# Optimization experiments

Measured on AMD Instinct MI355X. Metric: run time of the kernel, lower is better.

The kernel has to match this reference:

```python
import jax, jax.numpy as jnp
import numpy as np

B, S, D, H = 4, 2048, 1024, 16
HD = D // H

def setup_inputs() -> dict:
    key = jax.random.key(0)
    ks = jax.random.split(key, 11)
    s = 1.0 / np.sqrt(D)
    return {
        "q": jax.random.normal(ks[0], (B, S, D), jnp.float32),
        "k": jax.random.normal(ks[1], (B, S, D), jnp.float32),
        "v": jax.random.normal(ks[2], (B, S, D), jnp.float32),
        "Wq": jax.random.normal(ks[3], (D, D), jnp.float32) * s,
        "bq": jax.random.normal(ks[4], (D,), jnp.float32) * 0.01,
        "Wk": jax.random.normal(ks[5], (D, D), jnp.float32) * s,
        "bk": jax.random.normal(ks[6], (D,), jnp.float32) * 0.01,
        "Wv": jax.random.normal(ks[7], (D, D), jnp.float32) * s,
        "bv": jax.random.normal(ks[8], (D,), jnp.float32) * 0.01,
        "Wo": jax.random.normal(ks[9], (D, D), jnp.float32) * s,
        "bo": jax.random.normal(ks[10], (D,), jnp.float32) * 0.01,
    }

def reference(q, k, v, Wq, bq, Wk, bk, Wv, bv, Wo, bo):
    # linear projections + ReLU activation (as in the torch module)
    qh = jax.nn.relu(q @ Wq.T + bq)
    kh = jax.nn.relu(k @ Wk.T + bk)
    vh = jax.nn.relu(v @ Wv.T + bv)
    # split heads: [B,S,D] -> [B,H,S,HD]
    def split(x):
        return x.reshape(B, S, H, HD).transpose(0, 2, 1, 3)
    qh, kh, vh = split(qh), split(kh), split(vh)
    scale = 1.0 / np.sqrt(HD).astype(np.float32)
    scores = jnp.einsum("bhqd,bhkd->bhqk", qh, kh) * scale
    attn = jax.nn.softmax(scores, axis=-1)
    y = jnp.einsum("bhqk,bhkd->bhqd", attn, vh)
    # merge heads: [B,H,S,HD] -> [B,S,D]
    y = y.transpose(0, 2, 1, 3).reshape(B, S, D)
    return jax.nn.relu(y @ Wo.T + bo)
```

## Files before the change

kernel.cpp:

```cpp
#include <hip/hip_runtime.h>
#include <hip/hip_bf16.h>
#include <cstdint>
#include <cstddef>

#define Bc 4
#define Sc 2048
#define Dc 1024
#define Hc 16

typedef __bf16 bf16;
typedef bf16  bf16x4 __attribute__((ext_vector_type(4)));
typedef bf16  bf16x8 __attribute__((ext_vector_type(8)));
typedef float f32x4  __attribute__((ext_vector_type(4)));

__device__ __forceinline__ void load_lds16(const bf16* g, bf16* l) {
    __builtin_amdgcn_global_load_lds((const __attribute__((address_space(1))) void*)g,
                                     (__attribute__((address_space(3))) void*)l,
                                     16, 0, 0);
}

__device__ __forceinline__ void cvt16(const float* __restrict__ g,
                                      bf16x8& lo, bf16x8& hi) {
    const f32x4 a0 = *(const f32x4*)(g);
    const f32x4 a1 = *(const f32x4*)(g + 4);
    const f32x4 a2 = *(const f32x4*)(g + 8);
    const f32x4 a3 = *(const f32x4*)(g + 12);
#pragma unroll
    for (int j = 0; j < 4; j++) {
        lo[j]     = (bf16)a0[j];
        lo[j + 4] = (bf16)a1[j];
        hi[j]     = (bf16)a2[j];
        hi[j + 4] = (bf16)a3[j];
    }
}

__device__ __forceinline__ void store_relu(float* p, float v) { *p = fmaxf(v, 0.0f); }
__device__ __forceinline__ void store_relu(bf16*  p, float v) { *p = (bf16)fmaxf(v, 0.0f); }

__global__ __launch_bounds__(256)
void cvt_f32_bf16(const float* __restrict__ src, bf16* __restrict__ dst, int n16) {
    const int idx = blockIdx.x * 256 + threadIdx.x;
    if (idx >= n16) return;
    bf16x8 lo, hi;
    cvt16(src + (size_t)idx * 16, lo, hi);
    *(bf16x8*)(dst + (size_t)idx * 16)     = lo;
    *(bf16x8*)(dst + (size_t)idx * 16 + 8) = hi;
}

__global__ __launch_bounds__(256)
void cvt_w4(const float* __restrict__ s0, const float* __restrict__ s1,
            const float* __restrict__ s2, const float* __restrict__ s3,
            bf16* __restrict__ dst) {
    const float* srcs[4] = {s0, s1, s2, s3};
    const float* src = srcs[blockIdx.y];
    const int idx = blockIdx.x * 256 + threadIdx.x;
    bf16x8 lo, hi;
    cvt16(src + (size_t)idx * 16, lo, hi);
    bf16* d = dst + (size_t)blockIdx.y * ((size_t)Dc * Dc) + (size_t)idx * 16;
    *(bf16x8*)d       = lo;
    *(bf16x8*)(d + 8) = hi;
}

#define BM 128
#define BN 64
#define BK 64

template <typename TC, bool TR>
__global__ __launch_bounds__(256)
void gemm_bb(const bf16* __restrict__ A, const bf16* __restrict__ W,
             const float* __restrict__ bias, TC* __restrict__ C,
             int M, int N, int K) {
    __shared__ __align__(16) char pool[24576];
    bf16* lA = (bf16*)pool;
    bf16* lB = (bf16*)(pool + 16384);

    const int t    = threadIdx.x;
    const int lane = t & 63;
    const int wave = t >> 6;
    const int l15  = lane & 15;
    const int quad = lane >> 4;

    const int m0 = blockIdx.x * BM;
    const int n0 = blockIdx.y * BN;
    const int wm = (wave >> 1) * 64;
    const int wn = (wave & 1) * 32;

    f32x4 acc[4][2] = {};

    const int srow = t >> 3;
    const int cg   = (((t & 7) ^ (srow & 7)) << 3);
    const bf16* gA = A + (size_t)(m0 + srow) * K + cg;
    const bf16* gW = W + (size_t)(n0 + srow) * K + cg;
    bf16* lA0 = lA + t * 8;
    bf16* lB0 = lB + t * 8;

    for (int k0 = 0; k0 < K; k0 += BK) {
        __syncthreads();
#pragma unroll
        for (int c = 0; c < 4; c++)
            load_lds16(gA + (size_t)(32 * c) * K, lA0 + c * 2048);
#pragma unroll
        for (int c = 0; c < 2; c++)
            load_lds16(gW + (size_t)(32 * c) * K, lB0 + c * 2048);
        gA += BK; gW += BK;
        __syncthreads();

#pragma unroll
        for (int ks = 0; ks < 2; ks++) {
            bf16x8 af[4], bfr[2];
            const int colp = ((((ks << 2) | quad) ^ (l15 & 7)) << 3);
#pragma unroll
            for (int mt = 0; mt < 4; mt++) {
                const int row = wm + mt * 16 + l15;
                af[mt] = *(const bf16x8*)(lA + row * BK + colp);
            }
#pragma unroll
            for (int nt = 0; nt < 2; nt++) {
                const int row = wn + nt * 16 + l15;
                bfr[nt] = *(const bf16x8*)(lB + row * BK + colp);
            }
#pragma unroll
            for (int mt = 0; mt < 4; mt++)
#pragma unroll
                for (int nt = 0; nt < 2; nt++)
                    acc[mt][nt] = __builtin_amdgcn_mfma_f32_16x16x32_bf16(
                        af[mt], bfr[nt], acc[mt][nt], 0, 0, 0);
        }
    }

    if constexpr (!TR) {
#pragma unroll
        for (int nt = 0; nt < 2; nt++) {
            const int col = n0 + wn + nt * 16 + l15;
            const float bv = bias[col];
#pragma unroll
            for (int mt = 0; mt < 4; mt++) {
                const int rowb = m0 + wm + mt * 16 + quad * 4;
#pragma unroll
                for (int i = 0; i < 4; i++)
                    store_relu(&C[(size_t)(rowb + i) * N + col], acc[mt][nt][i] + bv);
            }
        }
    } else {
        __syncthreads();
        bf16* trp = (bf16*)pool;
#pragma unroll
        for (int nt = 0; nt < 2; nt++) {
            const int col = n0 + wn + nt * 16 + l15;
            const float bv = bias[col];
#pragma unroll
            for (int mt = 0; mt < 4; mt++)
#pragma unroll
                for (int i = 0; i < 4; i++)
                    trp[((wave * 32) + nt * 16 + l15) * 72 + mt * 16 + quad * 4 + i] =
                        (bf16)fmaxf(acc[mt][nt][i] + bv, 0.0f);
        }
        __syncthreads();
        const int r2 = lane >> 3;
        const int c8 = (lane & 7) * 8;
#pragma unroll
        for (int rr = 0; rr < 4; rr++) {
            const int rt = rr * 8 + r2;
            const bf16x8 vv = *(const bf16x8*)&trp[((wave * 32) + rt) * 72 + c8];
            const int cg2 = n0 + wn + rt;
            const int h   = cg2 >> 6, hd = cg2 & 63;
            const int mg  = m0 + wm + c8;
            const int b   = mg >> 11, s = mg & (Sc - 1);
            bf16* dst = (bf16*)C + ((size_t)(b * Hc + h) * 64 + hd) * Sc + s;
            *(bf16x8*)dst = vv;
        }
    }
}

#define QI 4

__global__ __launch_bounds__(256)
void attn_flash(const bf16* __restrict__ Qh, const bf16* __restrict__ Kh,
                const bf16* __restrict__ Vt_g, bf16* __restrict__ Y) {
    __shared__ __align__(16) bf16 Kl[64][72];
    __shared__ __align__(16) bf16 Vl[64][72];
    __shared__ __align__(16) bf16 Pl[4][64][72];

    const int t    = threadIdx.x;
    const int lane = t & 63;
    const int wave = t >> 6;
    const int l15  = lane & 15;
    const int quad = lane >> 4;

    const int bh = blockIdx.x;
    const int qt = blockIdx.y;
    const int b  = bh >> 4;
    const int h  = bh & 15;
    const int q0 = qt * 256;
    const size_t rowbase = (size_t)b * Sc;
    const size_t vhead   = (size_t)(b * Hc + h) * 64;

    const float qscale = 0.125f * 1.44269504f;
    bf16x8 qf[QI][2];
#pragma unroll
    for (int qi = 0; qi < QI; qi++) {
        const bf16* qp = Qh + (rowbase + q0 + wave * 64 + qi * 16 + l15) * (size_t)Dc + h * 64;
#pragma unroll
        for (int ks = 0; ks < 2; ks++) {
            const bf16x8 raw = *(const bf16x8*)(qp + ks * 32 + quad * 8);
#pragma unroll
            for (int j = 0; j < 8; j++) qf[qi][ks][j] = (bf16)((float)raw[j] * qscale);
        }
    }

    bf16x8 ones;
#pragma unroll
    for (int j = 0; j < 8; j++) ones[j] = (bf16)1.0f;

    f32x4 yacc[QI][4] = {};
    f32x4 sacc[QI]    = {};

    const int sr = t >> 2;
    const int sc = (t & 3) * 16;
    constexpr int NT = Sc / 64;

    const bf16* kp = Kh + (rowbase + sr) * (size_t)Dc + h * 64 + sc;
    const bf16* vp = Vt_g + (vhead + sr) * (size_t)Sc + sc;
    bf16x8 k0 = *(const bf16x8*)kp;
    bf16x8 k1 = *(const bf16x8*)(kp + 8);
    bf16x8 v0 = *(const bf16x8*)vp;
    bf16x8 v1 = *(const bf16x8*)(vp + 8);

    for (int kt = 0; kt < NT; kt++) {
        __syncthreads();
        *(bf16x8*)&Kl[sr][sc]     = k0;
        *(bf16x8*)&Kl[sr][sc + 8] = k1;
        *(bf16x8*)&Vl[sr][sc]     = v0;
        *(bf16x8*)&Vl[sr][sc + 8] = v1;
        __syncthreads();

        if (kt + 1 < NT) {
            kp += (size_t)64 * Dc;
            vp += 64;
            k0 = *(const bf16x8*)kp;
            k1 = *(const bf16x8*)(kp + 8);
            v0 = *(const bf16x8*)vp;
            v1 = *(const bf16x8*)(vp + 8);
        }

        bf16x8 kf[4][2];
#pragma unroll
        for (int mt = 0; mt < 4; mt++) {
            kf[mt][0] = *(const bf16x8*)&Kl[mt * 16 + l15][quad * 8];
            kf[mt][1] = *(const bf16x8*)&Kl[mt * 16 + l15][32 + quad * 8];
        }

#pragma unroll
        for (int qi = 0; qi < QI; qi++) {
            f32x4 s[4];
            __builtin_amdgcn_s_setprio(1);
#pragma unroll
            for (int mt = 0; mt < 4; mt++) {
                s[mt] = (f32x4){0.f, 0.f, 0.f, 0.f};
                s[mt] = __builtin_amdgcn_mfma_f32_16x16x32_bf16(
                    kf[mt][0], qf[qi][0], s[mt], 0, 0, 0);
                s[mt] = __builtin_amdgcn_mfma_f32_16x16x32_bf16(
                    kf[mt][1], qf[qi][1], s[mt], 0, 0, 0);
            }
            __builtin_amdgcn_s_setprio(0);
#pragma unroll
            for (int mt = 0; mt < 4; mt++) {
                bf16x4 pk;
#pragma unroll
                for (int i = 0; i < 4; i++)
                    pk[i] = (bf16)__builtin_amdgcn_exp2f(s[mt][i]);
                *(bf16x4*)&Pl[wave][qi * 16 + l15][mt * 16 + quad * 4] = pk;
            }
        }

        bf16x8 vf[4][2];
#pragma unroll
        for (int nt = 0; nt < 4; nt++) {
            vf[nt][0] = *(const bf16x8*)&Vl[nt * 16 + l15][quad * 8];
            vf[nt][1] = *(const bf16x8*)&Vl[nt * 16 + l15][32 + quad * 8];
        }

        bf16x8 pf[QI][2];
#pragma unroll
        for (int qi = 0; qi < QI; qi++) {
            pf[qi][0] = *(const bf16x8*)&Pl[wave][qi * 16 + l15][quad * 8];
            pf[qi][1] = *(const bf16x8*)&Pl[wave][qi * 16 + l15][32 + quad * 8];
        }
        __builtin_amdgcn_s_setprio(1);
#pragma unroll
        for (int qi = 0; qi < QI; qi++) {
            sacc[qi] = __builtin_amdgcn_mfma_f32_16x16x32_bf16(ones, pf[qi][0], sacc[qi], 0, 0, 0);
            sacc[qi] = __builtin_amdgcn_mfma_f32_16x16x32_bf16(ones, pf[qi][1], sacc[qi], 0, 0, 0);
#pragma unroll
            for (int nt = 0; nt < 4; nt++) {
                yacc[qi][nt] = __builtin_amdgcn_mfma_f32_16x16x32_bf16(
                    vf[nt][0], pf[qi][0], yacc[qi][nt], 0, 0, 0);
                yacc[qi][nt] = __builtin_amdgcn_mfma_f32_16x16x32_bf16(
                    vf[nt][1], pf[qi][1], yacc[qi][nt], 0, 0, 0);
            }
        }
        __builtin_amdgcn_s_setprio(0);
    }

#pragma unroll
    for (int qi = 0; qi < QI; qi++) {
        const float inv = 1.0f / sacc[qi][0];
        bf16* yp = Y + (rowbase + q0 + wave * 64 + qi * 16 + l15) * (size_t)Dc + h * 64;
#pragma unroll
        for (int nt = 0; nt < 4; nt++)
#pragma unroll
            for (int i = 0; i < 4; i++)
                yp[nt * 16 + quad * 4 + i] = (bf16)(yacc[qi][nt][i] * inv);
    }
}

extern "C" void kernel_launch(void* const* d_in, const int* in_sizes, int n_in,
                              void* d_out, int out_size, void* d_ws, size_t ws_size,
                              hipStream_t stream) {
    const float* q  = (const float*)d_in[0];
    const float* k  = (const float*)d_in[1];
    const float* v  = (const float*)d_in[2];
    const float* Wq = (const float*)d_in[3];
    const float* bq = (const float*)d_in[4];
    const float* Wk = (const float*)d_in[5];
    const float* bk = (const float*)d_in[6];
    const float* Wv = (const float*)d_in[7];
    const float* bv = (const float*)d_in[8];
    const float* Wo = (const float*)d_in[9];
    const float* bo = (const float*)d_in[10];
    float* out = (float*)d_out;

    const int M = Bc * Sc;
    const int N = Dc;
    const int K = Dc;
    const size_t E  = (size_t)Bc * Sc * Dc;
    const size_t EW = (size_t)Dc * Dc;

    bf16* Qh   = (bf16*)d_out;
    bf16* Kh   = Qh + E;
    bf16* tmpA = (bf16*)d_ws;
    bf16* VtG  = tmpA + E;
    bf16* Wqb  = VtG + E;
    bf16* Wkb  = Wqb + EW;
    bf16* Wvb  = Wkb + EW;
    bf16* Wob  = Wvb + EW;

    const int n16  = (int)(E / 16);
    const int n16w = (int)(EW / 16);
    dim3 gc(n16 / 256);
    dim3 gw4(n16w / 256, 4);
    dim3 gg(M / BM, N / BN);
    dim3 ga(Bc * Hc, Sc / 256);

    cvt_w4<<<gw4, 256, 0, stream>>>(Wq, Wk, Wv, Wo, Wqb);

    cvt_f32_bf16<<<gc, 256, 0, stream>>>(q, tmpA, n16);
    gemm_bb<bf16, false><<<gg, 256, 0, stream>>>(tmpA, Wqb, bq, Qh, M, N, K);

    cvt_f32_bf16<<<gc, 256, 0, stream>>>(k, tmpA, n16);
    gemm_bb<bf16, false><<<gg, 256, 0, stream>>>(tmpA, Wkb, bk, Kh, M, N, K);

    cvt_f32_bf16<<<gc, 256, 0, stream>>>(v, tmpA, n16);
    gemm_bb<bf16, true><<<gg, 256, 0, stream>>>(tmpA, Wvb, bv, VtG, M, N, K);

    attn_flash<<<ga, 256, 0, stream>>>(Qh, Kh, VtG, tmpA);

    gemm_bb<float, false><<<gg, 256, 0, stream>>>(tmpA, Wob, bo, out, M, N, K);
}
```

Before: 376.9 us.

## Fuse fp32-to-bf16 input conversion into projection GEMM A-tile loads

Removes the three standalone conversion kernels for q, k and v. The projection GEMMs now read fp32 activations directly, converting them to bf16 in registers before writing to LDS. A register prefetch of the next A tile overlaps global loads with the current tile's MFMA work. In exchange, each GEMM reads twice as many A bytes and replaces the async global-to-LDS copy with register-staged stores, which adds register pressure.

```diff
diff --git a/kernel.cpp b/kernel.cpp
--- a/kernel.cpp
+++ b/kernel.cpp
@@ -36,16 +36,6 @@
 
 __device__ __forceinline__ void store_relu(float* p, float v) { *p = fmaxf(v, 0.0f); }
 __device__ __forceinline__ void store_relu(bf16*  p, float v) { *p = (bf16)fmaxf(v, 0.0f); }
-
-__global__ __launch_bounds__(256)
-void cvt_f32_bf16(const float* __restrict__ src, bf16* __restrict__ dst, int n16) {
-    const int idx = blockIdx.x * 256 + threadIdx.x;
-    if (idx >= n16) return;
-    bf16x8 lo, hi;
-    cvt16(src + (size_t)idx * 16, lo, hi);
-    *(bf16x8*)(dst + (size_t)idx * 16)     = lo;
-    *(bf16x8*)(dst + (size_t)idx * 16 + 8) = hi;
-}
 
 __global__ __launch_bounds__(256)
 void cvt_w4(const float* __restrict__ s0, const float* __restrict__ s1,
@@ -65,9 +55,9 @@
 #define BN 64
 #define BK 64
 
-template <typename TC, bool TR>
+template <typename TC, bool TR, bool AF32>
 __global__ __launch_bounds__(256)
-void gemm_bb(const bf16* __restrict__ A, const bf16* __restrict__ W,
+void gemm_bb(const void* __restrict__ Av, const bf16* __restrict__ W,
              const float* __restrict__ bias, TC* __restrict__ C,
              int M, int N, int K) {
     __shared__ __align__(16) char pool[24576];
@@ -89,21 +79,57 @@
 
     const int srow = t >> 3;
     const int cg   = (((t & 7) ^ (srow & 7)) << 3);
-    const bf16* gA = A + (size_t)(m0 + srow) * K + cg;
+    const bf16*  gAb = (const bf16*)Av + (size_t)(m0 + srow) * K + cg;
+    const float* gAf = (const float*)Av + (size_t)(m0 + srow) * K + cg;
     const bf16* gW = W + (size_t)(n0 + srow) * K + cg;
     bf16* lA0 = lA + t * 8;
     bf16* lB0 = lB + t * 8;
 
+    f32x4 pre[8];
+    if constexpr (AF32) {
+#pragma unroll
+        for (int c = 0; c < 4; c++) {
+            const float* p = gAf + (size_t)(32 * c) * K;
+            pre[2 * c]     = *(const f32x4*)p;
+            pre[2 * c + 1] = *(const f32x4*)(p + 4);
+        }
+    }
+
     for (int k0 = 0; k0 < K; k0 += BK) {
         __syncthreads();
-#pragma unroll
-        for (int c = 0; c < 4; c++)
-            load_lds16(gA + (size_t)(32 * c) * K, lA0 + c * 2048);
+        if constexpr (AF32) {
+#pragma unroll
+            for (int c = 0; c < 4; c++) {
+                bf16x8 w;
+#pragma unroll
+                for (int j = 0; j < 4; j++) {
+                    w[j]     = (bf16)pre[2 * c][j];
+                    w[j + 4] = (bf16)pre[2 * c + 1][j];
+                }
+                *(bf16x8*)(lA0 + c * 2048) = w;
+            }
+        } else {
+#pragma unroll
+            for (int c = 0; c < 4; c++)
+                load_lds16(gAb + (size_t)(32 * c) * K + k0, lA0 + c * 2048);
+        }
 #pragma unroll
         for (int c = 0; c < 2; c++)
             load_lds16(gW + (size_t)(32 * c) * K, lB0 + c * 2048);
-        gA += BK; gW += BK;
-        __syncthreads();
+        gW += BK;
+        __syncthreads();
+
+        if constexpr (AF32) {
+            if (k0 + BK < K) {
+                const float* nA = gAf + (k0 + BK);
+#pragma unroll
+                for (int c = 0; c < 4; c++) {
+                    const float* p = nA + (size_t)(32 * c) * K;
+                    pre[2 * c]     = *(const f32x4*)p;
+                    pre[2 * c + 1] = *(const f32x4*)(p + 4);
+                }
+            }
+        }
 
 #pragma unroll
         for (int ks = 0; ks < 2; ks++) {
@@ -345,25 +371,18 @@
     bf16* Wvb  = Wkb + EW;
     bf16* Wob  = Wvb + EW;
 
-    const int n16  = (int)(E / 16);
     const int n16w = (int)(EW / 16);
-    dim3 gc(n16 / 256);
     dim3 gw4(n16w / 256, 4);
     dim3 gg(M / BM, N / BN);
     dim3 ga(Bc * Hc, Sc / 256);
 
     cvt_w4<<<gw4, 256, 0, stream>>>(Wq, Wk, Wv, Wo, Wqb);
 
-    cvt_f32_bf16<<<gc, 256, 0, stream>>>(q, tmpA, n16);
-    gemm_bb<bf16, false><<<gg, 256, 0, stream>>>(tmpA, Wqb, bq, Qh, M, N, K);
-
-    cvt_f32_bf16<<<gc, 256, 0, stream>>>(k, tmpA, n16);
-    gemm_bb<bf16, false><<<gg, 256, 0, stream>>>(tmpA, Wkb, bk, Kh, M, N, K);
-
-    cvt_f32_bf16<<<gc, 256, 0, stream>>>(v, tmpA, n16);
-    gemm_bb<bf16, true><<<gg, 256, 0, stream>>>(tmpA, Wvb, bv, VtG, M, N, K);
+    gemm_bb<bf16, false, true><<<gg, 256, 0, stream>>>(q, Wqb, bq, Qh, M, N, K);
+    gemm_bb<bf16, false, true><<<gg, 256, 0, stream>>>(k, Wkb, bk, Kh, M, N, K);
+    gemm_bb<bf16, true,  true><<<gg, 256, 0, stream>>>(v, Wvb, bv, VtG, M, N, K);
 
     attn_flash<<<ga, 256, 0, stream>>>(Qh, Kh, VtG, tmpA);
 
-    gemm_bb<float, false><<<gg, 256, 0, stream>>>(tmpA, Wob, bo, out, M, N, K);
-}
+    gemm_bb<float, false, false><<<gg, 256, 0, stream>>>(tmpA, Wob, bo, out, M, N, K);
+}
```

New measurement: 382.7 us. Within noise of the previous version (+1.6%).
